# Kernel tuning notes

Measured on AMD Instinct MI355X. Metric: run time of the kernel, lower is better.

The kernel has to match this reference:

```python
import jax, jax.numpy as jnp
import numpy as np

NEG_SLOPE = 0.2
EPS = 1e-16
N_NODES = 50000
N_EDGES = 800000
D_IN = 128
D_E = 64
HEADS = 4
D_OUT = 32


def setup_inputs() -> dict:
    key = jax.random.key(0)
    k1, k2, k3, k4, k5, k6 = jax.random.split(key, 6)
    H = jax.random.normal(k1, (N_NODES, D_IN), dtype=jnp.float32)
    edge_index = jax.random.randint(k2, (2, N_EDGES), 0, N_NODES, dtype=jnp.int64)
    E = jax.random.normal(k3, (N_EDGES, D_E), dtype=jnp.float32)
    # torch nn.Linear weights: [out_features, in_features]
    W = jax.random.normal(k4, (HEADS * D_OUT, D_IN), dtype=jnp.float32) * (1.0 / np.sqrt(D_IN))
    W_e = jax.random.normal(k5, (HEADS * D_OUT, D_E), dtype=jnp.float32) * (1.0 / np.sqrt(D_E))
    att = jax.random.normal(k6, (1, HEADS, D_OUT), dtype=jnp.float32) * 0.1
    return {"H": H, "edge_index": edge_index, "E": E, "W": W, "W_e": W_e, "att": att}


def reference(H, edge_index, E, W, W_e, att):
    n_nodes = H.shape[0]
    # node transform: [N, heads, d_out]
    HT = (H @ W.T).reshape(n_nodes, HEADS, D_OUT)
    src, dst = edge_index[0], edge_index[1]
    # edge transform: [E, heads, d_out]
    ET = (E @ W_e.T).reshape(-1, HEADS, D_OUT)
    alpha_in = HT[src] + HT[dst] + ET              # [E, heads, d_out]
    alpha_in = jax.nn.leaky_relu(alpha_in, NEG_SLOPE)
    alpha = jnp.sum(alpha_in * att, axis=-1)        # [E, heads]
    # segment softmax over incoming edges of each dst node
    a_max = jax.ops.segment_max(alpha, dst, num_segments=n_nodes)   # [N, heads]
    alpha = jnp.exp(alpha - a_max[dst])
    a_sum = jax.ops.segment_sum(alpha, dst, num_segments=n_nodes)   # [N, heads]
    alpha = alpha / (a_sum[dst] + EPS)
    # weighted aggregation of source features
    messages = HT[src] * alpha[:, :, None]          # [E, heads, d_out]
    H_out = jax.ops.segment_sum(messages, dst, num_segments=n_nodes)  # [N, heads, d_out]
    return H_out.reshape(n_nodes, HEADS * D_OUT)    # concat=True
```

## Files before the change

### kernel.cpp

```cpp
#include <hip/hip_runtime.h>

#define N_NODES 50000
#define N_EDGES 800000
#define D_IN    128
#define D_E     64
#define NH      4
#define F_TOT   128
#define NEG_SLOPE 0.2f

typedef __attribute__((ext_vector_type(8))) short short8;
typedef __attribute__((ext_vector_type(4))) float f32x4;

__device__ __forceinline__ short f2bf(float x) {
    unsigned u = __float_as_uint(x);
    u += 0x7FFFu + ((u >> 16) & 1u);
    return (short)(u >> 16);
}

__global__ __launch_bounds__(256) void k_node_transform(
    const float* __restrict__ H, const float* __restrict__ W,
    float* __restrict__ HT)
{
    __shared__ float wt[D_IN * F_TOT];
    const int tid = threadIdx.x;
    for (int i = tid; i < D_IN * F_TOT; i += 256) {
        const int f = i & 127, k = i >> 7;
        wt[k * F_TOT + f] = W[f * D_IN + k];
    }
    __syncthreads();

    const int l = tid & 63;
    const int w = tid >> 6;
    const int gwave  = blockIdx.x * 4 + w;
    const int nwaves = gridDim.x * 4;
    const int ngroups = N_NODES / 8;

    for (int grp = gwave; grp < ngroups; grp += nwaves) {
        const int g = grp * 8;
        float ax[8], ay[8];
#pragma unroll
        for (int j = 0; j < 8; ++j) { ax[j] = 0.f; ay[j] = 0.f; }

        for (int k4 = 0; k4 < D_IN / 4; ++k4) {
            float hv[8][4];
#pragma unroll
            for (int j = 0; j < 8; ++j)
                *(float4*)hv[j] = *(const float4*)&H[(size_t)(g + j) * D_IN + k4 * 4];
#pragma unroll
            for (int kk = 0; kk < 4; ++kk) {
                const float2 wk = *(const float2*)&wt[(k4 * 4 + kk) * F_TOT + 2 * l];
#pragma unroll
                for (int j = 0; j < 8; ++j) {
                    ax[j] = fmaf(wk.x, hv[j][kk], ax[j]);
                    ay[j] = fmaf(wk.y, hv[j][kk], ay[j]);
                }
            }
        }
#pragma unroll
        for (int j = 0; j < 8; ++j) {
            float2 r; r.x = ax[j]; r.y = ay[j];
            *(float2*)&HT[(size_t)(g + j) * F_TOT + 2 * l] = r;
        }
    }
}

__global__ __launch_bounds__(256) void k_hist(
    const int* __restrict__ EI, int* __restrict__ deg)
{
    const int e = blockIdx.x * 256 + threadIdx.x;
    if (e < N_EDGES) atomicAdd(&deg[EI[N_EDGES + e]], 1);
}

__global__ __launch_bounds__(1024) void k_scan(
    const int* __restrict__ deg, int* __restrict__ row_start,
    int* __restrict__ cursor)
{
    __shared__ int wsum[16];
    __shared__ int carry;
    const int tid = threadIdx.x;
    const int l = tid & 63;
    const int wv = tid >> 6;
    if (tid == 0) carry = 0;

    for (int base = 0; base < N_NODES; base += 1024) {
        __syncthreads();
        const int cb = carry;
        const int i = base + tid;
        const int v = (i < N_NODES) ? deg[i] : 0;
        int x = v;
#pragma unroll
        for (int off = 1; off < 64; off <<= 1) {
            int t = __shfl_up(x, off, 64);
            if (l >= off) x += t;
        }
        if (l == 63) wsum[wv] = x;
        __syncthreads();
        int wave_off = 0;
        for (int k = 0; k < wv; ++k) wave_off += wsum[k];
        int tot = 0;
#pragma unroll
        for (int k = 0; k < 16; ++k) tot += wsum[k];
        const int excl = cb + wave_off + (x - v);
        if (i < N_NODES) { row_start[i] = excl; cursor[i] = excl; }
        __syncthreads();
        if (tid == 0) carry = cb + tot;
    }
    __syncthreads();
    if (tid == 0) row_start[N_NODES] = carry;
}

__global__ __launch_bounds__(256) void k_permute(
    const int* __restrict__ EI, int* __restrict__ cursor,
    int2* __restrict__ perm)
{
    const int e = blockIdx.x * 256 + threadIdx.x;
    if (e < N_EDGES) {
        const int src = EI[e];
        const int dst = EI[N_EDGES + e];
        const int pos = atomicAdd(&cursor[dst], 1);
        perm[pos] = make_int2(e, src);
    }
}

__global__ __launch_bounds__(256, 2) void k_fused(
    const float* __restrict__ E, const float* __restrict__ We,
    const float* __restrict__ att, const float* __restrict__ HT,
    const int2* __restrict__ perm, const int* __restrict__ row_start,
    float* __restrict__ out)
{
    __shared__ short8 s_bf[8][2][64];
    __shared__ f32x4  s_att[8][4];
    __shared__ f32x4  s_hd[4][8][4];

    const int tid = threadIdx.x;
    const int l   = tid & 63;
    const int wv  = tid >> 6;
    const int r16 = l & 15;
    const int g4  = l >> 4;

    if (wv == 0) {
#pragma unroll
        for (int ft = 0; ft < 8; ++ft) {
#pragma unroll
            for (int kc = 0; kc < 2; ++kc) {
                const float* wp = &We[(size_t)(ft * 16 + r16) * D_E + kc * 32 + g4 * 8];
                const f32x4 lo = *(const f32x4*)wp;
                const f32x4 hi = *(const f32x4*)(wp + 4);
                short8 b;
                b[0] = f2bf(lo[0]); b[1] = f2bf(lo[1]); b[2] = f2bf(lo[2]); b[3] = f2bf(lo[3]);
                b[4] = f2bf(hi[0]); b[5] = f2bf(hi[1]); b[6] = f2bf(hi[2]); b[7] = f2bf(hi[3]);
                s_bf[ft][kc][l] = b;
            }
        }
        if (l < 32) {
            const int ft = l >> 2, g = l & 3;
            s_att[ft][g] = *(const f32x4*)&att[ft * 16 + g * 4];
        }
    }
    __syncthreads();

    const int gw      = blockIdx.x * 4 + wv;
    const int gstride = gridDim.x * 4;

    for (int n = gw; n < N_NODES; n += gstride) {
        const int beg = row_start[n];
        const int end = row_start[n + 1];

        if (l < 32)
            s_hd[wv][l >> 2][l & 3] = *(const f32x4*)&HT[(size_t)n * F_TOT + l * 4];

        f32x4 am[8];
#pragma unroll
        for (int ft = 0; ft < 8; ++ft) am[ft] = (f32x4){0.f, 0.f, 0.f, 0.f};
        float sw[4] = {0.f, 0.f, 0.f, 0.f};

        for (int t = beg; t < end; t += 16) {
            const int  idx   = t + r16;
            const bool valid = idx < end;
            const int2 pe    = perm[valid ? idx : end - 1];
            const int  eid   = pe.x;
            const int  sr    = pe.y;

            const float* hsp = &HT[(size_t)sr * F_TOT + g4 * 4];
            f32x4 hs4[8];
#pragma unroll
            for (int ft = 0; ft < 8; ++ft)
                hs4[ft] = *(const f32x4*)(hsp + ft * 16);

            short8 af[2];
#pragma unroll
            for (int kc = 0; kc < 2; ++kc) {
                const float* ep = &E[(size_t)eid * D_E + kc * 32 + g4 * 8];
                const f32x4 lo = *(const f32x4*)ep;
                const f32x4 hi = *(const f32x4*)(ep + 4);
                short8 a;
                a[0] = f2bf(lo[0]); a[1] = f2bf(lo[1]); a[2] = f2bf(lo[2]); a[3] = f2bf(lo[3]);
                a[4] = f2bf(hi[0]); a[5] = f2bf(hi[1]); a[6] = f2bf(hi[2]); a[7] = f2bf(hi[3]);
                af[kc] = a;
            }

            float ph[4] = {0.f, 0.f, 0.f, 0.f};
#pragma unroll
            for (int ft = 0; ft < 8; ++ft) {
                f32x4 z = {0.f, 0.f, 0.f, 0.f};
                z = __builtin_amdgcn_mfma_f32_16x16x32_bf16(s_bf[ft][0][l], af[0], z, 0, 0, 0);
                const f32x4 acc =
                    __builtin_amdgcn_mfma_f32_16x16x32_bf16(s_bf[ft][1][l], af[1], z, 0, 0, 0);
                const f32x4 at = s_att[ft][g4];
                const f32x4 hd = s_hd[wv][ft][g4];
#pragma unroll
                for (int r = 0; r < 4; ++r) {
                    float v = hs4[ft][r] + hd[r] + acc[r];
                    v = v > 0.f ? v : NEG_SLOPE * v;
                    ph[ft >> 1] = fmaf(v, at[r], ph[ft >> 1]);
                }
            }
#pragma unroll
            for (int h = 0; h < 4; ++h) {
                ph[h] += __shfl_xor(ph[h], 16, 64);
                ph[h] += __shfl_xor(ph[h], 32, 64);
            }
            float w[4];
#pragma unroll
            for (int h = 0; h < 4; ++h) {
                w[h] = valid ? __expf(ph[h]) : 0.f;
                sw[h] += w[h];
            }
#pragma unroll
            for (int ft = 0; ft < 8; ++ft) {
                const float wh = w[ft >> 1];
#pragma unroll
                for (int r = 0; r < 4; ++r)
                    am[ft][r] = fmaf(wh, hs4[ft][r], am[ft][r]);
            }
        }

#pragma unroll
        for (int m = 1; m < 16; m <<= 1) {
#pragma unroll
            for (int h = 0; h < 4; ++h) sw[h] += __shfl_xor(sw[h], m, 64);
#pragma unroll
            for (int ft = 0; ft < 8; ++ft)
#pragma unroll
                for (int r = 0; r < 4; ++r)
                    am[ft][r] += __shfl_xor(am[ft][r], m, 64);
        }
        float inv[4];
#pragma unroll
        for (int h = 0; h < 4; ++h) inv[h] = 1.f / (sw[h] + 1e-16f);

        if (r16 == 0) {
#pragma unroll
            for (int ft = 0; ft < 8; ++ft) {
                f32x4 o;
#pragma unroll
                for (int r = 0; r < 4; ++r) o[r] = am[ft][r] * inv[ft >> 1];
                *(f32x4*)&out[(size_t)n * F_TOT + ft * 16 + g4 * 4] = o;
            }
        }
    }
}

extern "C" void kernel_launch(void* const* d_in, const int* in_sizes, int n_in,
                              void* d_out, int out_size, void* d_ws, size_t ws_size,
                              hipStream_t stream)
{
    const float* H   = (const float*)d_in[0];
    const int*   EI  = (const int*)d_in[1];
    const float* E   = (const float*)d_in[2];
    const float* W   = (const float*)d_in[3];
    const float* We  = (const float*)d_in[4];
    const float* att = (const float*)d_in[5];
    float* out = (float*)d_out;

    float* HT        = (float*)d_ws;
    int2*  perm      = (int2*)(HT + (size_t)N_NODES * F_TOT);
    int*   deg       = (int*)(perm + N_EDGES);
    int*   row_start = deg + N_NODES;
    int*   cursor    = row_start + N_NODES + 1;

    hipMemsetAsync(deg, 0, N_NODES * sizeof(int), stream);

    k_hist<<<(N_EDGES + 255) / 256, 256, 0, stream>>>(EI, deg);
    k_scan<<<1, 1024, 0, stream>>>(deg, row_start, cursor);
    k_node_transform<<<512, 256, 0, stream>>>(H, W, HT);
    k_permute<<<(N_EDGES + 255) / 256, 256, 0, stream>>>(EI, cursor, perm);
    k_fused<<<1024, 256, 0, stream>>>(E, We, att, HT, perm, row_start, out);
}
```

Measured before the change: 661.6 us.

## Fuse histogram into node transform, vectorize scan, double-tile edge loop

Merges the degree histogram into the node-transform kernel to save a launch. Rewrites the single-block scan to read int4 and combine wave sums with shuffles instead of serial loops. Processes edges in pairs of 16-edge tiles, issuing the gathers for both tiles before computing either, to raise memory-level parallelism. This costs more registers in the fused kernel, which could hurt occupancy.

```diff
diff --git a/kernel.cpp b/kernel.cpp
--- a/kernel.cpp
+++ b/kernel.cpp
@@ -17,12 +17,16 @@
     return (short)(u >> 16);
 }
 
-__global__ __launch_bounds__(256) void k_node_transform(
+__global__ __launch_bounds__(256) void k_pre(
     const float* __restrict__ H, const float* __restrict__ W,
-    float* __restrict__ HT)
-{
+    float* __restrict__ HT, const int* __restrict__ EI,
+    int* __restrict__ deg)
+{
+    const int tid = threadIdx.x;
+    for (int e = blockIdx.x * 256 + tid; e < N_EDGES; e += gridDim.x * 256)
+        atomicAdd(&deg[EI[N_EDGES + e]], 1);
+
     __shared__ float wt[D_IN * F_TOT];
-    const int tid = threadIdx.x;
     for (int i = tid; i < D_IN * F_TOT; i += 256) {
         const int f = i & 127, k = i >> 7;
         wt[k * F_TOT + f] = W[f * D_IN + k];
@@ -62,13 +66,6 @@
             *(float2*)&HT[(size_t)(g + j) * F_TOT + 2 * l] = r;
         }
     }
-}
-
-__global__ __launch_bounds__(256) void k_hist(
-    const int* __restrict__ EI, int* __restrict__ deg)
-{
-    const int e = blockIdx.x * 256 + threadIdx.x;
-    if (e < N_EDGES) atomicAdd(&deg[EI[N_EDGES + e]], 1);
 }
 
 __global__ __launch_bounds__(1024) void k_scan(
@@ -82,12 +79,17 @@
     const int wv = tid >> 6;
     if (tid == 0) carry = 0;
 
-    for (int base = 0; base < N_NODES; base += 1024) {
+    const int4* deg4 = (const int4*)deg;
+    const int N4 = N_NODES / 4;
+
+    for (int base = 0; base < N4; base += 1024) {
         __syncthreads();
         const int cb = carry;
-        const int i = base + tid;
-        const int v = (i < N_NODES) ? deg[i] : 0;
-        int x = v;
+        const int i4 = base + tid;
+        int4 d = make_int4(0, 0, 0, 0);
+        if (i4 < N4) d = deg4[i4];
+        const int t0 = d.x, t1 = t0 + d.y, t2 = t1 + d.z, t3 = t2 + d.w;
+        int x = t3;
 #pragma unroll
         for (int off = 1; off < 64; off <<= 1) {
             int t = __shfl_up(x, off, 64);
@@ -95,14 +97,21 @@
         }
         if (l == 63) wsum[wv] = x;
         __syncthreads();
-        int wave_off = 0;
-        for (int k = 0; k < wv; ++k) wave_off += wsum[k];
-        int tot = 0;
-#pragma unroll
-        for (int k = 0; k < 16; ++k) tot += wsum[k];
-        const int excl = cb + wave_off + (x - v);
-        if (i < N_NODES) { row_start[i] = excl; cursor[i] = excl; }
-        __syncthreads();
+        int s = (l < 16) ? wsum[l] : 0;
+#pragma unroll
+        for (int off = 1; off < 16; off <<= 1) {
+            int t = __shfl_up(s, off, 64);
+            if (l >= off) s += t;
+        }
+        const int tot      = __shfl(s, 15, 64);
+        const int wave_off = (wv == 0) ? 0 : __shfl(s, wv - 1, 64);
+        const int excl     = cb + wave_off + (x - t3);
+        if (i4 < N4) {
+            int4 rs;
+            rs.x = excl; rs.y = excl + t0; rs.z = excl + t1; rs.w = excl + t2;
+            ((int4*)row_start)[i4] = rs;
+            ((int4*)cursor)[i4]    = rs;
+        }
         if (tid == 0) carry = cb + tot;
     }
     __syncthreads();
@@ -121,6 +130,69 @@
         perm[pos] = make_int2(e, src);
     }
 }
+
+
+#define TILE_LOADRAW(PE, HS, E0, E1, E2, E3)                                  \
+    {                                                                         \
+        const float* hsp_ = &HT[(size_t)(PE).y * F_TOT + g4 * 4];             \
+        _Pragma("unroll")                                                     \
+        for (int ft = 0; ft < 8; ++ft)                                        \
+            HS[ft] = *(const f32x4*)(hsp_ + ft * 16);                         \
+        const float* ep_ = &E[(size_t)(PE).x * D_E + g4 * 8];                 \
+        E0 = *(const f32x4*)ep_;                                              \
+        E1 = *(const f32x4*)(ep_ + 4);                                        \
+        E2 = *(const f32x4*)(ep_ + 32);                                       \
+        E3 = *(const f32x4*)(ep_ + 36);                                       \
+    }
+
+#define TILE_CONV(E0, E1, E2, E3, AF)                                         \
+    {                                                                         \
+        short8 a_;                                                            \
+        a_[0]=f2bf(E0[0]); a_[1]=f2bf(E0[1]); a_[2]=f2bf(E0[2]); a_[3]=f2bf(E0[3]); \
+        a_[4]=f2bf(E1[0]); a_[5]=f2bf(E1[1]); a_[6]=f2bf(E1[2]); a_[7]=f2bf(E1[3]); \
+        AF[0] = a_;                                                           \
+        a_[0]=f2bf(E2[0]); a_[1]=f2bf(E2[1]); a_[2]=f2bf(E2[2]); a_[3]=f2bf(E2[3]); \
+        a_[4]=f2bf(E3[0]); a_[5]=f2bf(E3[1]); a_[6]=f2bf(E3[2]); a_[7]=f2bf(E3[3]); \
+        AF[1] = a_;                                                           \
+    }
+
+#define TILE_COMPUTE(HS, AF, VMASK)                                           \
+    {                                                                         \
+        float ph_[4] = {0.f, 0.f, 0.f, 0.f};                                  \
+        _Pragma("unroll")                                                     \
+        for (int ft = 0; ft < 8; ++ft) {                                      \
+            f32x4 z_ = {0.f, 0.f, 0.f, 0.f};                                  \
+            z_ = __builtin_amdgcn_mfma_f32_16x16x32_bf16(s_bf[ft][0][l], AF[0], z_, 0, 0, 0); \
+            const f32x4 acc_ =                                                \
+                __builtin_amdgcn_mfma_f32_16x16x32_bf16(s_bf[ft][1][l], AF[1], z_, 0, 0, 0);  \
+            const f32x4 at_ = s_att[ft][g4];                                  \
+            const f32x4 hd_ = s_hd[wv][ft][g4];                               \
+            _Pragma("unroll")                                                 \
+            for (int r = 0; r < 4; ++r) {                                     \
+                float v_ = HS[ft][r] + hd_[r] + acc_[r];                      \
+                v_ = v_ > 0.f ? v_ : NEG_SLOPE * v_;                          \
+                ph_[ft >> 1] = fmaf(v_, at_[r], ph_[ft >> 1]);                \
+            }                                                                 \
+        }                                                                     \
+        _Pragma("unroll")                                                     \
+        for (int h = 0; h < 4; ++h) {                                         \
+            ph_[h] += __shfl_xor(ph_[h], 16, 64);                             \
+            ph_[h] += __shfl_xor(ph_[h], 32, 64);                             \
+        }                                                                     \
+        float w4_[4];                                                         \
+        _Pragma("unroll")                                                     \
+        for (int h = 0; h < 4; ++h) {                                         \
+            w4_[h] = (VMASK) ? __expf(ph_[h]) : 0.f;                          \
+            sw[h] += w4_[h];                                                  \
+        }                                                                     \
+        _Pragma("unroll")                                                     \
+        for (int ft = 0; ft < 8; ++ft) {                                      \
+            const float wh_ = w4_[ft >> 1];                                   \
+            _Pragma("unroll")                                                 \
+            for (int r = 0; r < 4; ++r)                                       \
+                am[ft][r] = fmaf(wh_, HS[ft][r], am[ft][r]);                  \
+        }                                                                     \
+    }
 
 __global__ __launch_bounds__(256, 2) void k_fused(
     const float* __restrict__ E, const float* __restrict__ We,
@@ -174,64 +246,33 @@
         for (int ft = 0; ft < 8; ++ft) am[ft] = (f32x4){0.f, 0.f, 0.f, 0.f};
         float sw[4] = {0.f, 0.f, 0.f, 0.f};
 
-        for (int t = beg; t < end; t += 16) {
-            const int  idx   = t + r16;
-            const bool valid = idx < end;
-            const int2 pe    = perm[valid ? idx : end - 1];
-            const int  eid   = pe.x;
-            const int  sr    = pe.y;
-
-            const float* hsp = &HT[(size_t)sr * F_TOT + g4 * 4];
-            f32x4 hs4[8];
-#pragma unroll
-            for (int ft = 0; ft < 8; ++ft)
-                hs4[ft] = *(const f32x4*)(hsp + ft * 16);
-
-            short8 af[2];
-#pragma unroll
-            for (int kc = 0; kc < 2; ++kc) {
-                const float* ep = &E[(size_t)eid * D_E + kc * 32 + g4 * 8];
-                const f32x4 lo = *(const f32x4*)ep;
-                const f32x4 hi = *(const f32x4*)(ep + 4);
-                short8 a;
-                a[0] = f2bf(lo[0]); a[1] = f2bf(lo[1]); a[2] = f2bf(lo[2]); a[3] = f2bf(lo[3]);
-                a[4] = f2bf(hi[0]); a[5] = f2bf(hi[1]); a[6] = f2bf(hi[2]); a[7] = f2bf(hi[3]);
-                af[kc] = a;
-            }
-
-            float ph[4] = {0.f, 0.f, 0.f, 0.f};
-#pragma unroll
-            for (int ft = 0; ft < 8; ++ft) {
-                f32x4 z = {0.f, 0.f, 0.f, 0.f};
-                z = __builtin_amdgcn_mfma_f32_16x16x32_bf16(s_bf[ft][0][l], af[0], z, 0, 0, 0);
-                const f32x4 acc =
-                    __builtin_amdgcn_mfma_f32_16x16x32_bf16(s_bf[ft][1][l], af[1], z, 0, 0, 0);
-                const f32x4 at = s_att[ft][g4];
-                const f32x4 hd = s_hd[wv][ft][g4];
-#pragma unroll
-                for (int r = 0; r < 4; ++r) {
-                    float v = hs4[ft][r] + hd[r] + acc[r];
-                    v = v > 0.f ? v : NEG_SLOPE * v;
-                    ph[ft >> 1] = fmaf(v, at[r], ph[ft >> 1]);
-                }
-            }
-#pragma unroll
-            for (int h = 0; h < 4; ++h) {
-                ph[h] += __shfl_xor(ph[h], 16, 64);
-                ph[h] += __shfl_xor(ph[h], 32, 64);
-            }
-            float w[4];
-#pragma unroll
-            for (int h = 0; h < 4; ++h) {
-                w[h] = valid ? __expf(ph[h]) : 0.f;
-                sw[h] += w[h];
-            }
-#pragma unroll
-            for (int ft = 0; ft < 8; ++ft) {
-                const float wh = w[ft >> 1];
-#pragma unroll
-                for (int r = 0; r < 4; ++r)
-                    am[ft][r] = fmaf(wh, hs4[ft][r], am[ft][r]);
+        for (int t = beg; t < end; t += 32) {
+            const int  iA = t + r16;
+            const bool vA = iA < end;
+            const int2 peA = perm[vA ? iA : end - 1];
+            const bool anyB = (t + 16) < end;
+
+            f32x4 hsA[8], eA0, eA1, eA2, eA3;
+            short8 afA[2];
+            f32x4 hsB[8], eB0, eB1, eB2, eB3;
+            short8 afB[2];
+            int2 peB;
+
+            TILE_LOADRAW(peA, hsA, eA0, eA1, eA2, eA3);
+            if (anyB) {
+                const int  iB = t + 16 + r16;
+                const bool vB_ = iB < end;
+                peB = perm[vB_ ? iB : end - 1];
+                TILE_LOADRAW(peB, hsB, eB0, eB1, eB2, eB3);
+            }
+
+            TILE_CONV(eA0, eA1, eA2, eA3, afA);
+            TILE_COMPUTE(hsA, afA, vA);
+
+            if (anyB) {
+                const bool vB = (t + 16 + r16) < end;
+                TILE_CONV(eB0, eB1, eB2, eB3, afB);
+                TILE_COMPUTE(hsB, afB, vB);
             }
         }
 
@@ -277,13 +318,12 @@
     int2*  perm      = (int2*)(HT + (size_t)N_NODES * F_TOT);
     int*   deg       = (int*)(perm + N_EDGES);
     int*   row_start = deg + N_NODES;
-    int*   cursor    = row_start + N_NODES + 1;
+    int*   cursor    = row_start + N_NODES + 4;
 
     hipMemsetAsync(deg, 0, N_NODES * sizeof(int), stream);
 
-    k_hist<<<(N_EDGES + 255) / 256, 256, 0, stream>>>(EI, deg);
+    k_pre<<<512, 256, 0, stream>>>(H, W, HT, EI, deg);
     k_scan<<<1, 1024, 0, stream>>>(deg, row_start, cursor);
-    k_node_transform<<<512, 256, 0, stream>>>(H, W, HT);
     k_permute<<<(N_EDGES + 255) / 256, 256, 0, stream>>>(EI, cursor, perm);
     k_fused<<<1024, 256, 0, stream>>>(E, We, att, HT, perm, row_start, out);
 }
```

After: 761.6 us. 1.15x slower.

## Software-pipeline fused edge loop across nodes, merge histogram into transform, vectorize scan

Applied to the files above, without the earlier changes.

The fused aggregation kernel becomes a flattened, software-pipelined loop over 16-edge chunks that spans node boundaries. Perm entries are prefetched two chunks ahead and E rows and source HT rows one chunk ahead, so gather latency overlaps with MFMA and softmax work. The degree histogram is merged into the node-transform kernel to remove a launch, and the scan now reads and writes int4 and uses a shuffle-based wave-offset scan. In exchange the code adds more registers and control complexity, plus a safety iteration cap on the loop.

```diff
diff --git a/kernel.cpp b/kernel.cpp
--- a/kernel.cpp
+++ b/kernel.cpp
@@ -17,12 +17,20 @@
     return (short)(u >> 16);
 }
 
-__global__ __launch_bounds__(256) void k_node_transform(
+__device__ __forceinline__ int rfl(int x) {
+    return __builtin_amdgcn_readfirstlane(x);
+}
+
+__global__ __launch_bounds__(256) void k_pre(
     const float* __restrict__ H, const float* __restrict__ W,
-    float* __restrict__ HT)
-{
+    float* __restrict__ HT, const int* __restrict__ EI,
+    int* __restrict__ deg)
+{
+    const int tid = threadIdx.x;
+    for (int e = blockIdx.x * 256 + tid; e < N_EDGES; e += gridDim.x * 256)
+        atomicAdd(&deg[EI[N_EDGES + e]], 1);
+
     __shared__ float wt[D_IN * F_TOT];
-    const int tid = threadIdx.x;
     for (int i = tid; i < D_IN * F_TOT; i += 256) {
         const int f = i & 127, k = i >> 7;
         wt[k * F_TOT + f] = W[f * D_IN + k];
@@ -62,13 +70,6 @@
             *(float2*)&HT[(size_t)(g + j) * F_TOT + 2 * l] = r;
         }
     }
-}
-
-__global__ __launch_bounds__(256) void k_hist(
-    const int* __restrict__ EI, int* __restrict__ deg)
-{
-    const int e = blockIdx.x * 256 + threadIdx.x;
-    if (e < N_EDGES) atomicAdd(&deg[EI[N_EDGES + e]], 1);
 }
 
 __global__ __launch_bounds__(1024) void k_scan(
@@ -82,12 +83,17 @@
     const int wv = tid >> 6;
     if (tid == 0) carry = 0;
 
-    for (int base = 0; base < N_NODES; base += 1024) {
+    const int4* deg4 = (const int4*)deg;
+    const int N4 = N_NODES / 4;
+
+    for (int base = 0; base < N4; base += 1024) {
         __syncthreads();
         const int cb = carry;
-        const int i = base + tid;
-        const int v = (i < N_NODES) ? deg[i] : 0;
-        int x = v;
+        const int i4 = base + tid;
+        int4 d = make_int4(0, 0, 0, 0);
+        if (i4 < N4) d = deg4[i4];
+        const int t0 = d.x, t1 = t0 + d.y, t2 = t1 + d.z, t3 = t2 + d.w;
+        int x = t3;
 #pragma unroll
         for (int off = 1; off < 64; off <<= 1) {
             int t = __shfl_up(x, off, 64);
@@ -95,14 +101,21 @@
         }
         if (l == 63) wsum[wv] = x;
         __syncthreads();
-        int wave_off = 0;
-        for (int k = 0; k < wv; ++k) wave_off += wsum[k];
-        int tot = 0;
-#pragma unroll
-        for (int k = 0; k < 16; ++k) tot += wsum[k];
-        const int excl = cb + wave_off + (x - v);
-        if (i < N_NODES) { row_start[i] = excl; cursor[i] = excl; }
-        __syncthreads();
+        int s = (l < 16) ? wsum[l] : 0;
+#pragma unroll
+        for (int off = 1; off < 16; off <<= 1) {
+            int t = __shfl_up(s, off, 64);
+            if (l >= off) s += t;
+        }
+        const int tot      = __shfl(s, 15, 64);
+        const int wave_off = (wv == 0) ? 0 : __shfl(s, wv - 1, 64);
+        const int excl     = cb + wave_off + (x - t3);
+        if (i4 < N4) {
+            int4 rs;
+            rs.x = excl; rs.y = excl + t0; rs.z = excl + t1; rs.w = excl + t2;
+            ((int4*)row_start)[i4] = rs;
+            ((int4*)cursor)[i4]    = rs;
+        }
         if (tid == 0) carry = cb + tot;
     }
     __syncthreads();
@@ -159,106 +172,159 @@
     }
     __syncthreads();
 
-    const int gw      = blockIdx.x * 4 + wv;
-    const int gstride = gridDim.x * 4;
-
-    for (int n = gw; n < N_NODES; n += gstride) {
-        const int beg = row_start[n];
-        const int end = row_start[n + 1];
-
-        if (l < 32)
-            s_hd[wv][l >> 2][l & 3] = *(const f32x4*)&HT[(size_t)n * F_TOT + l * 4];
-
-        f32x4 am[8];
-#pragma unroll
-        for (int ft = 0; ft < 8; ++ft) am[ft] = (f32x4){0.f, 0.f, 0.f, 0.f};
-        float sw[4] = {0.f, 0.f, 0.f, 0.f};
-
-        for (int t = beg; t < end; t += 16) {
-            const int  idx   = t + r16;
-            const bool valid = idx < end;
-            const int2 pe    = perm[valid ? idx : end - 1];
-            const int  eid   = pe.x;
-            const int  sr    = pe.y;
-
-            const float* hsp = &HT[(size_t)sr * F_TOT + g4 * 4];
-            f32x4 hs4[8];
-#pragma unroll
-            for (int ft = 0; ft < 8; ++ft)
-                hs4[ft] = *(const f32x4*)(hsp + ft * 16);
-
-            short8 af[2];
-#pragma unroll
-            for (int kc = 0; kc < 2; ++kc) {
-                const float* ep = &E[(size_t)eid * D_E + kc * 32 + g4 * 8];
-                const f32x4 lo = *(const f32x4*)ep;
-                const f32x4 hi = *(const f32x4*)(ep + 4);
-                short8 a;
-                a[0] = f2bf(lo[0]); a[1] = f2bf(lo[1]); a[2] = f2bf(lo[2]); a[3] = f2bf(lo[3]);
-                a[4] = f2bf(hi[0]); a[5] = f2bf(hi[1]); a[6] = f2bf(hi[2]); a[7] = f2bf(hi[3]);
-                af[kc] = a;
-            }
-
-            float ph[4] = {0.f, 0.f, 0.f, 0.f};
-#pragma unroll
-            for (int ft = 0; ft < 8; ++ft) {
-                f32x4 z = {0.f, 0.f, 0.f, 0.f};
-                z = __builtin_amdgcn_mfma_f32_16x16x32_bf16(s_bf[ft][0][l], af[0], z, 0, 0, 0);
-                const f32x4 acc =
-                    __builtin_amdgcn_mfma_f32_16x16x32_bf16(s_bf[ft][1][l], af[1], z, 0, 0, 0);
-                const f32x4 at = s_att[ft][g4];
-                const f32x4 hd = s_hd[wv][ft][g4];
-#pragma unroll
-                for (int r = 0; r < 4; ++r) {
-                    float v = hs4[ft][r] + hd[r] + acc[r];
-                    v = v > 0.f ? v : NEG_SLOPE * v;
-                    ph[ft >> 1] = fmaf(v, at[r], ph[ft >> 1]);
+    const int gs = rfl(gridDim.x * 4);
+
+    int n0 = rfl(blockIdx.x * 4 + wv);
+    int t0 = rfl(row_start[n0]);
+    int e0 = rfl(row_start[n0 + 1]);
+
+    int n1 = n0, t1, e1;
+    if (t0 + 16 < e0) { t1 = t0 + 16; e1 = e0; }
+    else {
+        n1 = n0 + gs;
+        if (n1 < N_NODES) { t1 = rfl(row_start[n1]); e1 = rfl(row_start[n1 + 1]); }
+        else { t1 = 0; e1 = 0; }
+    }
+    int n2 = n1, t2, e2;
+    if (t1 + 16 < e1) { t2 = t1 + 16; e2 = e1; }
+    else if (n1 < N_NODES) {
+        n2 = n1 + gs;
+        if (n2 < N_NODES) { t2 = rfl(row_start[n2]); e2 = rfl(row_start[n2 + 1]); }
+        else { t2 = 0; e2 = 0; }
+    } else { t2 = 0; e2 = 0; }
+
+    int nN = n2 + gs;
+    int bN = 0, eN = 0;
+    if (nN < N_NODES) { bN = rfl(row_start[nN]); eN = rfl(row_start[nN + 1]); }
+
+#define PCLAMP(T, EE) (max(min((T) + r16, (EE) - 1), 0))
+
+    int2 pe0v = perm[PCLAMP(t0, e0)];
+    int2 pe1v = perm[PCLAMP(t1, e1)];
+    int2 pe2v = perm[PCLAMP(t2, e2)];
+
+    f32x4 ev0, ev1, ev2, ev3;
+    {
+        const float* ep = &E[(size_t)pe0v.x * D_E + g4 * 8];
+        ev0 = *(const f32x4*)ep;       ev1 = *(const f32x4*)(ep + 4);
+        ev2 = *(const f32x4*)(ep + 32); ev3 = *(const f32x4*)(ep + 36);
+    }
+    f32x4 hsv[8];
+    {
+        const float* hp = &HT[(size_t)pe0v.y * F_TOT + g4 * 4];
+#pragma unroll
+        for (int ft = 0; ft < 8; ++ft) hsv[ft] = *(const f32x4*)(hp + ft * 16);
+    }
+    if (l < 32 && n0 < N_NODES)
+        s_hd[wv][l >> 2][l & 3] = *(const f32x4*)&HT[(size_t)n0 * F_TOT + l * 4];
+
+    f32x4 am[8];
+#pragma unroll
+    for (int ft = 0; ft < 8; ++ft) am[ft] = (f32x4){0.f, 0.f, 0.f, 0.f};
+    float sw[4] = {0.f, 0.f, 0.f, 0.f};
+    f32x4 hdld = (f32x4){0.f, 0.f, 0.f, 0.f};
+
+    int safety = 65536;
+    while (n0 < N_NODES && safety-- > 0) {
+        int n2n = n2, t2n = t2, e2n = e2;
+        if (t2 + 16 < e2) { t2n = t2 + 16; }
+        else if (n2 < N_NODES) {
+            n2n = nN;
+            if (nN < N_NODES) { t2n = bN; e2n = eN; } else { t2n = 0; e2n = 0; }
+            nN += gs;
+            if (nN < N_NODES) { bN = rfl(row_start[nN]); eN = rfl(row_start[nN + 1]); }
+        }
+        int2 peT = perm[PCLAMP(t2n, e2n)];
+        if (l < 32 && n1 < N_NODES)
+            hdld = *(const f32x4*)&HT[(size_t)n1 * F_TOT + l * 4];
+
+        short8 af0, af1;
+        af0[0]=f2bf(ev0[0]); af0[1]=f2bf(ev0[1]); af0[2]=f2bf(ev0[2]); af0[3]=f2bf(ev0[3]);
+        af0[4]=f2bf(ev1[0]); af0[5]=f2bf(ev1[1]); af0[6]=f2bf(ev1[2]); af0[7]=f2bf(ev1[3]);
+        af1[0]=f2bf(ev2[0]); af1[1]=f2bf(ev2[1]); af1[2]=f2bf(ev2[2]); af1[3]=f2bf(ev2[3]);
+        af1[4]=f2bf(ev3[0]); af1[5]=f2bf(ev3[1]); af1[6]=f2bf(ev3[2]); af1[7]=f2bf(ev3[3]);
+        {
+            const float* ep = &E[(size_t)pe1v.x * D_E + g4 * 8];
+            ev0 = *(const f32x4*)ep;       ev1 = *(const f32x4*)(ep + 4);
+            ev2 = *(const f32x4*)(ep + 32); ev3 = *(const f32x4*)(ep + 36);
+        }
+
+        float ph[4] = {0.f, 0.f, 0.f, 0.f};
+#pragma unroll
+        for (int ft = 0; ft < 8; ++ft) {
+            f32x4 z = {0.f, 0.f, 0.f, 0.f};
+            z = __builtin_amdgcn_mfma_f32_16x16x32_bf16(s_bf[ft][0][l], af0, z, 0, 0, 0);
+            const f32x4 acc =
+                __builtin_amdgcn_mfma_f32_16x16x32_bf16(s_bf[ft][1][l], af1, z, 0, 0, 0);
+            const f32x4 at = s_att[ft][g4];
+            const f32x4 hd = s_hd[wv][ft][g4];
+#pragma unroll
+            for (int r = 0; r < 4; ++r) {
+                float v = hsv[ft][r] + hd[r] + acc[r];
+                v = v > 0.f ? v : NEG_SLOPE * v;
+                ph[ft >> 1] = fmaf(v, at[r], ph[ft >> 1]);
+            }
+        }
+        const bool valid = (t0 + r16) < e0;
+#pragma unroll
+        for (int h = 0; h < 4; ++h) {
+            ph[h] += __shfl_xor(ph[h], 16, 64);
+            ph[h] += __shfl_xor(ph[h], 32, 64);
+        }
+        float w[4];
+#pragma unroll
+        for (int h = 0; h < 4; ++h) {
+            w[h] = valid ? __expf(ph[h]) : 0.f;
+            sw[h] += w[h];
+        }
+#pragma unroll
+        for (int ft = 0; ft < 8; ++ft) {
+            const float wh = w[ft >> 1];
+#pragma unroll
+            for (int r = 0; r < 4; ++r)
+                am[ft][r] = fmaf(wh, hsv[ft][r], am[ft][r]);
+        }
+        {
+            const float* hp = &HT[(size_t)pe1v.y * F_TOT + g4 * 4];
+#pragma unroll
+            for (int ft = 0; ft < 8; ++ft) hsv[ft] = *(const f32x4*)(hp + ft * 16);
+        }
+
+        if (n1 != n0) {
+#pragma unroll
+            for (int m = 1; m < 16; m <<= 1) {
+#pragma unroll
+                for (int h = 0; h < 4; ++h) sw[h] += __shfl_xor(sw[h], m, 64);
+#pragma unroll
+                for (int ft = 0; ft < 8; ++ft)
+#pragma unroll
+                    for (int r = 0; r < 4; ++r)
+                        am[ft][r] += __shfl_xor(am[ft][r], m, 64);
+            }
+            float inv[4];
+#pragma unroll
+            for (int h = 0; h < 4; ++h) inv[h] = 1.f / (sw[h] + 1e-16f);
+            if (r16 == 0) {
+#pragma unroll
+                for (int ft = 0; ft < 8; ++ft) {
+                    f32x4 o;
+#pragma unroll
+                    for (int r = 0; r < 4; ++r) o[r] = am[ft][r] * inv[ft >> 1];
+                    *(f32x4*)&out[(size_t)n0 * F_TOT + ft * 16 + g4 * 4] = o;
                 }
             }
 #pragma unroll
-            for (int h = 0; h < 4; ++h) {
-                ph[h] += __shfl_xor(ph[h], 16, 64);
-                ph[h] += __shfl_xor(ph[h], 32, 64);
-            }
-            float w[4];
-#pragma unroll
-            for (int h = 0; h < 4; ++h) {
-                w[h] = valid ? __expf(ph[h]) : 0.f;
-                sw[h] += w[h];
-            }
-#pragma unroll
-            for (int ft = 0; ft < 8; ++ft) {
-                const float wh = w[ft >> 1];
-#pragma unroll
-                for (int r = 0; r < 4; ++r)
-                    am[ft][r] = fmaf(wh, hs4[ft][r], am[ft][r]);
-            }
-        }
-
-#pragma unroll
-        for (int m = 1; m < 16; m <<= 1) {
-#pragma unroll
-            for (int h = 0; h < 4; ++h) sw[h] += __shfl_xor(sw[h], m, 64);
-#pragma unroll
-            for (int ft = 0; ft < 8; ++ft)
-#pragma unroll
-                for (int r = 0; r < 4; ++r)
-                    am[ft][r] += __shfl_xor(am[ft][r], m, 64);
-        }
-        float inv[4];
-#pragma unroll
-        for (int h = 0; h < 4; ++h) inv[h] = 1.f / (sw[h] + 1e-16f);
-
-        if (r16 == 0) {
-#pragma unroll
-            for (int ft = 0; ft < 8; ++ft) {
-                f32x4 o;
-#pragma unroll
-                for (int r = 0; r < 4; ++r) o[r] = am[ft][r] * inv[ft >> 1];
-                *(f32x4*)&out[(size_t)n * F_TOT + ft * 16 + g4 * 4] = o;
-            }
-        }
-    }
+            for (int ft = 0; ft < 8; ++ft) am[ft] = (f32x4){0.f, 0.f, 0.f, 0.f};
+            sw[0] = sw[1] = sw[2] = sw[3] = 0.f;
+        }
+        if (l < 32) s_hd[wv][l >> 2][l & 3] = hdld;
+
+        n0 = n1; t0 = t1; e0 = e1;
+        n1 = n2; t1 = t2; e1 = e2;
+        n2 = n2n; t2 = t2n; e2 = e2n;
+        pe1v = pe2v; pe2v = peT;
+    }
+#undef PCLAMP
 }
 
 extern "C" void kernel_launch(void* const* d_in, const int* in_sizes, int n_in,
@@ -277,13 +343,12 @@
     int2*  perm      = (int2*)(HT + (size_t)N_NODES * F_TOT);
     int*   deg       = (int*)(perm + N_EDGES);
     int*   row_start = deg + N_NODES;
-    int*   cursor    = row_start + N_NODES + 1;
+    int*   cursor    = row_start + N_NODES + 4;
 
     hipMemsetAsync(deg, 0, N_NODES * sizeof(int), stream);
 
-    k_hist<<<(N_EDGES + 255) / 256, 256, 0, stream>>>(EI, deg);
+    k_pre<<<512, 256, 0, stream>>>(H, W, HT, EI, deg);
     k_scan<<<1, 1024, 0, stream>>>(deg, row_start, cursor);
-    k_node_transform<<<512, 256, 0, stream>>>(H, W, HT);
     k_permute<<<(N_EDGES + 255) / 256, 256, 0, stream>>>(EI, cursor, perm);
     k_fused<<<1024, 256, 0, stream>>>(E, We, att, HT, perm, row_start, out);
 }
```

Result: faster. 560.7 us (-15.2%).
